# Kernel optimization log

Hardware: AMD Instinct MI355X
Metric: run time of the kernel (lower is better)

The kernel has to match this reference:

```python
import jax, jax.numpy as jnp
import numpy as np

NUM_HEADS = 16
NUM_KV_HEADS = 4
HEAD_DIM = 128
ROPE_BASE = 10000.0


def _apply_rope(x):
    # x: [B, H, S, D], interleaved RoPE: x1 = x[..., ::2], x2 = x[..., 1::2]
    B, H, S, D = x.shape
    inv_freq = 1.0 / (ROPE_BASE ** (jnp.arange(0, D, 2, dtype=jnp.float32) / D))  # [D/2]
    t = jnp.arange(S, dtype=jnp.float32)
    freqs = t[:, None] * inv_freq[None, :]          # [S, D/2]
    cos = jnp.cos(freqs)[None, None]                # [1,1,S,D/2]
    sin = jnp.sin(freqs)[None, None]
    xr = x.reshape(B, H, S, D // 2, 2)
    x1, x2 = xr[..., 0], xr[..., 1]
    r1 = x1 * cos - x2 * sin
    r2 = x1 * sin + x2 * cos
    return jnp.stack([r1, r2], axis=-1).reshape(B, H, S, D)


def setup_inputs() -> dict:
    key = jax.random.key(0)
    ks = jax.random.split(key, 5)
    H = NUM_HEADS * HEAD_DIM          # 2048
    KV = NUM_KV_HEADS * HEAD_DIM      # 512
    std = 0.02
    return {
        "hidden_states": jax.random.normal(ks[0], (1, 4096, H), dtype=jnp.float32),
        "wq": jax.random.normal(ks[1], (H, H), dtype=jnp.float32) * std,
        "wk": jax.random.normal(ks[2], (H, KV), dtype=jnp.float32) * std,
        "wv": jax.random.normal(ks[3], (H, KV), dtype=jnp.float32) * std,
        "wo": jax.random.normal(ks[4], (H, H), dtype=jnp.float32) * std,
    }


def reference(hidden_states, wq, wk, wv, wo):
    B, S, H = hidden_states.shape
    nh, nkv, hd = NUM_HEADS, NUM_KV_HEADS, HEAD_DIM
    scale = 1.0 / np.sqrt(hd)

    q = (hidden_states @ wq).reshape(B, S, nh, hd).transpose(0, 2, 1, 3)   # [B,nh,S,hd]
    k = (hidden_states @ wk).reshape(B, S, nkv, hd).transpose(0, 2, 1, 3)  # [B,nkv,S,hd]
    v = (hidden_states @ wv).reshape(B, S, nkv, hd).transpose(0, 2, 1, 3)

    q = _apply_rope(q)
    k = _apply_rope(k)

    rep = nh // nkv
    k = jnp.repeat(k, rep, axis=1)  # GQA head repetition -> [B,nh,S,hd]
    v = jnp.repeat(v, rep, axis=1)

    scores = jnp.einsum("bhqd,bhkd->bhqk", q, k) * scale
    causal = jnp.tril(jnp.ones((S, S), dtype=bool))
    scores = jnp.where(causal[None, None], scores, jnp.float32(-1e30))
    probs = jax.nn.softmax(scores, axis=-1)
    attn = jnp.einsum("bhqk,bhkd->bhqd", probs, v)      # [B,nh,S,hd]
    attn = attn.transpose(0, 2, 1, 3).reshape(B, S, H)
    return attn @ wo
```

## Files before the change

kernel.cpp:

```cpp
#include <hip/hip_runtime.h>

typedef unsigned short u16;
typedef unsigned int u32;
typedef __bf16 bf16x8 __attribute__((ext_vector_type(8)));
typedef float f32x4 __attribute__((ext_vector_type(4)));
typedef float f32x16 __attribute__((ext_vector_type(16)));
typedef int v2i __attribute__((ext_vector_type(2)));

#define S_LEN 4096
#define HDIM 2048
#define KVDIM 512
#define N_HEADS 16
#define HEAD_D 128

__device__ __forceinline__ u16 f2bf(float f) {
  u32 u = __float_as_uint(f);
  u32 r = (u + 0x7FFFu + ((u >> 16) & 1u)) >> 16;
  return (u16)r;
}
__device__ __forceinline__ float bf2f(u16 h) {
  return __uint_as_float(((u32)h) << 16);
}
__device__ __forceinline__ float exp2_fast(float x) {
  float r;
  asm("v_exp_f32 %0, %1" : "=v"(r) : "v"(x));
  return r;
}
__device__ __forceinline__ u32 cvt_pk_bf16(float lo, float hi) {
  u32 r;
  asm("v_cvt_pk_bf16_f32 %0, %1, %2" : "=v"(r) : "v"(lo), "v"(hi));
  return r;
}
__device__ __forceinline__ void gload16(const u16* g, const u16* l) {
  __builtin_amdgcn_global_load_lds(
      (const __attribute__((address_space(1))) void*)g,
      (__attribute__((address_space(3))) void*)l, 16, 0, 0);
}

__global__ void k_prep(const float* __restrict__ in, u16* __restrict__ out,
                       float* __restrict__ cosT, float* __restrict__ sinT) {
  int b = blockIdx.x;
  int tid = threadIdx.x;
  if (b < 4096) {
    int i = b * 256 + tid;
    const float4* p = reinterpret_cast<const float4*>(in) + (size_t)i * 2;
    float4 a = p[0], c = p[1];
    u32 o0 = (u32)f2bf(a.x) | ((u32)f2bf(a.y) << 16);
    u32 o1 = (u32)f2bf(a.z) | ((u32)f2bf(a.w) << 16);
    u32 o2 = (u32)f2bf(c.x) | ((u32)f2bf(c.y) << 16);
    u32 o3 = (u32)f2bf(c.z) | ((u32)f2bf(c.w) << 16);
    reinterpret_cast<uint4*>(out)[i] = make_uint4(o0, o1, o2, o3);
  } else {
    int i = (b - 4096) * 256 + tid;
    int pos = i >> 6, f = i & 63;
    float inv = expf(-0.1439115683121279f * (float)f);
    float ang = (float)pos * inv;
    float s, c;
    sincosf(ang, &s, &c);
    cosT[i] = c;
    sinT[i] = s;
  }
}

__global__ void k_transpose_all(const float* __restrict__ wq, const float* __restrict__ wk,
                                const float* __restrict__ wv, const float* __restrict__ wo,
                                u16* __restrict__ WqT, u16* __restrict__ WkT,
                                u16* __restrict__ WvT, u16* __restrict__ WoT) {
  __shared__ float t[32][33];
  int b = blockIdx.x;
  const float* W;
  u16* Wt;
  int Kd, Nd, bx, by;
  if (b < 4096) {
    W = wq; Wt = WqT; Kd = HDIM; Nd = HDIM; bx = b & 63; by = b >> 6;
  } else if (b < 5120) {
    int r = b - 4096; W = wk; Wt = WkT; Kd = HDIM; Nd = KVDIM; bx = r & 15; by = r >> 4;
  } else if (b < 6144) {
    int r = b - 5120; W = wv; Wt = WvT; Kd = HDIM; Nd = KVDIM; bx = r & 15; by = r >> 4;
  } else {
    int r = b - 6144; W = wo; Wt = WoT; Kd = HDIM; Nd = HDIM; bx = r & 63; by = r >> 6;
  }
  int tx = threadIdx.x & 31, ty = threadIdx.x >> 5;
  int n = bx * 32 + tx;
  for (int j = ty; j < 32; j += 8)
    t[j][tx] = W[(size_t)(by * 32 + j) * Nd + n];
  __syncthreads();
  int k = by * 32 + tx;
  for (int j = ty; j < 32; j += 8)
    Wt[(size_t)(bx * 32 + j) * Kd + k] = f2bf(t[tx][j]);
}

__global__ void k_rope_all(u16* __restrict__ Qb, u16* __restrict__ Kb,
                           const float* __restrict__ cosT, const float* __restrict__ sinT) {
  int b = blockIdx.x;
  u16* X;
  int width, i;
  if (b < 4096) { X = Qb; width = HDIM; i = b * 256 + threadIdx.x; }
  else { X = Kb; width = KVDIM; i = (b - 4096) * 256 + threadIdx.x; }
  size_t idx = (size_t)i * 8;
  int row = (int)(idx / width);
  int col = (int)(idx - (size_t)row * width);
  int fi = (col & 127) >> 1;
  float4 c4 = *reinterpret_cast<const float4*>(&cosT[(row << 6) + fi]);
  float4 s4 = *reinterpret_cast<const float4*>(&sinT[(row << 6) + fi]);
  uint4 v = *reinterpret_cast<const uint4*>(&X[idx]);
  float cc[4] = {c4.x, c4.y, c4.z, c4.w};
  float ss[4] = {s4.x, s4.y, s4.z, s4.w};
  u32 w_[4] = {v.x, v.y, v.z, v.w};
  u32 r_[4];
#pragma unroll
  for (int p = 0; p < 4; ++p) {
    float x1 = bf2f((u16)(w_[p] & 0xffff));
    float x2 = bf2f((u16)(w_[p] >> 16));
    float r1 = x1 * cc[p] - x2 * ss[p];
    float r2 = x1 * ss[p] + x2 * cc[p];
    r_[p] = (u32)f2bf(r1) | ((u32)f2bf(r2) << 16);
  }
  *reinterpret_cast<uint4*>(&X[idx]) = make_uint4(r_[0], r_[1], r_[2], r_[3]);
}

__global__ __launch_bounds__(256) void k_gemm_qkv(
    const u16* __restrict__ A, const u16* __restrict__ WqT, const u16* __restrict__ WkT,
    const u16* __restrict__ WvT, u16* __restrict__ Qb, u16* __restrict__ Kb,
    u16* __restrict__ VTb) {
  const int Kd = HDIM, M = S_LEN;
  __shared__ __align__(16) u16 As[128 * 32];
  __shared__ __align__(16) u16 Bs[128 * 32];
  const int p = blockIdx.x;
  const int bmg = p & 7, r = p >> 3;
  const int bm = (bmg * 4 + (r & 3)) * 128;
  const int by = r >> 2;
  const u16* Bt;
  int bn, N, mode;
  if (by < 16) { Bt = WqT; bn = by * 128; N = HDIM; mode = 0; }
  else if (by < 20) { Bt = WkT; bn = (by - 16) * 128; N = KVDIM; mode = 1; }
  else { Bt = WvT; bn = (by - 20) * 128; N = KVDIM; mode = 2; }
  const int tid = threadIdx.x;
  const int lane = tid & 63;
  const int wid = tid >> 6;
  const int wr = (wid >> 1) * 64, wc = (wid & 1) * 64;
  const int lr = lane & 15, lhi = lane >> 4;
  const int srow = lane >> 2;
  const int skc = (lane & 3) * 8;
  f32x4 acc[4][4] = {};
  for (int k0 = 0; k0 < Kd; k0 += 32) {
#pragma unroll
    for (int it = 0; it < 2; ++it) {
      int rowbase = (it * 4 + wid) * 16;
      gload16(&A[(size_t)(bm + rowbase + srow) * Kd + k0 + skc], &As[rowbase * 32]);
      gload16(&Bt[(size_t)(bn + rowbase + srow) * Kd + k0 + skc], &Bs[rowbase * 32]);
    }
    __syncthreads();
    bf16x8 af[4], bfr[4];
#pragma unroll
    for (int m = 0; m < 4; ++m)
      af[m] = *reinterpret_cast<const bf16x8*>(&As[(wr + m * 16 + lr) * 32 + lhi * 8]);
#pragma unroll
    for (int n = 0; n < 4; ++n)
      bfr[n] = *reinterpret_cast<const bf16x8*>(&Bs[(wc + n * 16 + lr) * 32 + lhi * 8]);
#pragma unroll
    for (int m = 0; m < 4; ++m)
#pragma unroll
      for (int n = 0; n < 4; ++n)
        acc[m][n] = __builtin_amdgcn_mfma_f32_16x16x32_bf16(af[m], bfr[n], acc[m][n], 0, 0, 0);
    __syncthreads();
  }
#pragma unroll
  for (int m = 0; m < 4; ++m) {
    int grow0 = bm + wr + m * 16 + lhi * 4;
#pragma unroll
    for (int n = 0; n < 4; ++n) {
      int gcol = bn + wc + n * 16 + lr;
      if (mode == 2) {
        ushort4 pk;
        pk.x = f2bf(acc[m][n][0]);
        pk.y = f2bf(acc[m][n][1]);
        pk.z = f2bf(acc[m][n][2]);
        pk.w = f2bf(acc[m][n][3]);
        *reinterpret_cast<ushort4*>(&VTb[(size_t)gcol * M + grow0]) = pk;
      } else {
        u16* outp = (mode == 0) ? Qb : Kb;
#pragma unroll
        for (int r2 = 0; r2 < 4; ++r2)
          outp[(size_t)(grow0 + r2) * N + gcol] = f2bf(acc[m][n][r2]);
      }
    }
  }
}

__global__ __launch_bounds__(256) void k_gemm_bt(
    const u16* __restrict__ A, const u16* __restrict__ Bt, float* __restrict__ Cout,
    int M, int N, int Kd) {
  __shared__ __align__(16) u16 As[128 * 32];
  __shared__ __align__(16) u16 Bs[128 * 32];
  const int p = blockIdx.x;
  const int bmg = p & 7, r = p >> 3;
  const int bm = (bmg * 4 + (r & 3)) * 128;
  const int bn = (r >> 2) * 128;
  const int tid = threadIdx.x;
  const int lane = tid & 63;
  const int wid = tid >> 6;
  const int wr = (wid >> 1) * 64, wc = (wid & 1) * 64;
  const int lr = lane & 15, lhi = lane >> 4;
  const int srow = lane >> 2;
  const int skc = (lane & 3) * 8;
  f32x4 acc[4][4] = {};
  for (int k0 = 0; k0 < Kd; k0 += 32) {
#pragma unroll
    for (int it = 0; it < 2; ++it) {
      int rowbase = (it * 4 + wid) * 16;
      gload16(&A[(size_t)(bm + rowbase + srow) * Kd + k0 + skc], &As[rowbase * 32]);
      gload16(&Bt[(size_t)(bn + rowbase + srow) * Kd + k0 + skc], &Bs[rowbase * 32]);
    }
    __syncthreads();
    bf16x8 af[4], bfr[4];
#pragma unroll
    for (int m = 0; m < 4; ++m)
      af[m] = *reinterpret_cast<const bf16x8*>(&As[(wr + m * 16 + lr) * 32 + lhi * 8]);
#pragma unroll
    for (int n = 0; n < 4; ++n)
      bfr[n] = *reinterpret_cast<const bf16x8*>(&Bs[(wc + n * 16 + lr) * 32 + lhi * 8]);
#pragma unroll
    for (int m = 0; m < 4; ++m)
#pragma unroll
      for (int n = 0; n < 4; ++n)
        acc[m][n] = __builtin_amdgcn_mfma_f32_16x16x32_bf16(af[m], bfr[n], acc[m][n], 0, 0, 0);
    __syncthreads();
  }
#pragma unroll
  for (int m = 0; m < 4; ++m) {
    int grow0 = bm + wr + m * 16 + lhi * 4;
#pragma unroll
    for (int n = 0; n < 4; ++n) {
      int gcol = bn + wc + n * 16 + lr;
#pragma unroll
      for (int r2 = 0; r2 < 4; ++r2)
        Cout[(size_t)(grow0 + r2) * N + gcol] = acc[m][n][r2];
    }
  }
}

__global__ __launch_bounds__(256, 2) void k_attn(
    const u16* __restrict__ Q, const u16* __restrict__ K, const u16* __restrict__ VT,
    u16* __restrict__ PO0, u16* __restrict__ PO1, float2* __restrict__ ML) {
  __shared__ __align__(16) u16 Ks[64 * 128];
  __shared__ __align__(16) u16 Vs[128 * 64];
  int i = blockIdx.x;
  const int x = i & 7, s = i >> 3;
  const int kvh = x >> 1;
  const int kvhalf = x & 1;
  const int hp = s & 3;
  const int u = s >> 2;
  const int g = u & 7, jq = u >> 3;
  int qt;
  if (jq == 0) qt = g;
  else if (jq == 1) qt = 15 - g;
  else if (jq == 2) qt = 16 + g;
  else qt = 31 - g;
  const int h = kvh * 4 + hp;
  const int tid = threadIdx.x, lane = tid & 63, wid = tid >> 6;
  const int l31 = lane & 31, hi = lane >> 5;
  const int qw = qt * 128 + wid * 32;
  const int qglob = qw + l31;
  const float CE = 0.12751743f;
  const float THR = 62.74f;

  const u16* qptr = &Q[(size_t)qglob * HDIM + h * HEAD_D];
  bf16x8 qf[8];
#pragma unroll
  for (int ks = 0; ks < 8; ++ks)
    qf[ks] = *reinterpret_cast<const bf16x8*>(&qptr[ks * 16 + hi * 8]);

  f32x16 o_[4] = {};
  float m_ = -3e38f, l_ = 0.f;
  char* KsB = (char*)Ks;
  char* VsB = (char*)Vs;

  const int j0 = kvhalf * (qt + 1);
  const int j1 = j0 + qt + 1;
  for (int j = j0; j < j1; ++j) {
    const int kb = j << 6;
    __syncthreads();
#pragma unroll
    for (int it = 0; it < 4; ++it) {
      int sI = it * 256 + tid;
      int kv = sI >> 4, c16 = sI & 15;
      int db = kv * 256 + c16 * 16;
      db ^= ((db >> 8) & 7) << 4;
      *reinterpret_cast<uint4*>(KsB + db) = *reinterpret_cast<const uint4*>(
          &K[(size_t)(kb + kv) * KVDIM + kvh * HEAD_D + c16 * 8]);
    }
#pragma unroll
    for (int it = 0; it < 4; ++it) {
      int sI = it * 256 + tid;
      int d = sI >> 3, k16 = sI & 7;
      int db = d * 128 + k16 * 16;
      db ^= ((db >> 7) & 7) << 4;
      *reinterpret_cast<uint4*>(VsB + db) = *reinterpret_cast<const uint4*>(
          &VT[(size_t)(kvh * HEAD_D + d) * S_LEN + kb + k16 * 8]);
    }
    __syncthreads();

    if (kb <= qw + 31) {
      f32x16 s0 = {}, s1 = {};
#pragma unroll
      for (int ks = 0; ks < 8; ++ks) {
        int db0 = l31 * 256 + ks * 32 + hi * 16;
        db0 ^= ((db0 >> 8) & 7) << 4;
        int db1 = (32 + l31) * 256 + ks * 32 + hi * 16;
        db1 ^= ((db1 >> 8) & 7) << 4;
        bf16x8 k0 = *reinterpret_cast<const bf16x8*>(KsB + db0);
        bf16x8 k1 = *reinterpret_cast<const bf16x8*>(KsB + db1);
        s0 = __builtin_amdgcn_mfma_f32_32x32x16_bf16(k0, qf[ks], s0, 0, 0, 0);
        s1 = __builtin_amdgcn_mfma_f32_32x32x16_bf16(k1, qf[ks], s1, 0, 0, 0);
      }
      if (kb + 63 > qw) {
#pragma unroll
        for (int r = 0; r < 16; ++r) {
          int kvr = kb + (r & 3) + 8 * (r >> 2) + 4 * hi;
          if (kvr > qglob) s0[r] = -1e30f;
          if (kvr + 32 > qglob) s1[r] = -1e30f;
        }
      }
      float pm = fmaxf(s0[0], s1[0]);
#pragma unroll
      for (int r = 1; r < 16; ++r) pm = fmaxf(pm, fmaxf(s0[r], s1[r]));
      pm = fmaxf(pm, __shfl_xor(pm, 32));
      if (!__all(pm <= m_ + THR)) {
        float mnew = fmaxf(m_, pm);
        float fac = exp2_fast((m_ - mnew) * CE);
        m_ = mnew;
        l_ *= fac;
#pragma unroll
        for (int dt = 0; dt < 4; ++dt)
#pragma unroll
          for (int r = 0; r < 16; ++r) o_[dt][r] *= fac;
      }
      const float mc = m_ * CE;
      float rs = 0.f;
#pragma unroll
      for (int r = 0; r < 16; ++r) {
        s0[r] = exp2_fast(__builtin_fmaf(s0[r], CE, -mc));
        s1[r] = exp2_fast(__builtin_fmaf(s1[r], CE, -mc));
        rs += s0[r] + s1[r];
      }
      rs += __shfl_xor(rs, 32);
      l_ += rs;
#pragma unroll
      for (int kvt = 0; kvt < 2; ++kvt) {
        u32 xw[8], yw[8];
#pragma unroll
        for (int gI = 0; gI < 8; ++gI) {
          float plo = kvt ? s1[2 * gI] : s0[2 * gI];
          float phi = kvt ? s1[2 * gI + 1] : s0[2 * gI + 1];
          u32 pw = cvt_pk_bf16(plo, phi);
          v2i sw = __builtin_amdgcn_permlane32_swap((int)pw, (int)pw, false, false);
          xw[gI] = (u32)sw[0];
          yw[gI] = (u32)sw[1];
        }
#pragma unroll
        for (int ksl = 0; ksl < 2; ++ksl) {
          int b = ksl * 4;
          u32 f0 = hi ? xw[b + 2] : xw[b + 0];
          u32 f1 = hi ? xw[b + 3] : xw[b + 1];
          u32 f2 = hi ? yw[b + 2] : yw[b + 0];
          u32 f3 = hi ? yw[b + 3] : yw[b + 1];
          uint4 fr = make_uint4(f0, f1, f2, f3);
          bf16x8 pf = *reinterpret_cast<bf16x8*>(&fr);
          const int kvstep = kvt * 2 + ksl;
#pragma unroll
          for (int dt = 0; dt < 4; ++dt) {
            int db = (dt * 32 + l31) * 128 + kvstep * 32 + hi * 16;
            db ^= ((db >> 7) & 7) << 4;
            bf16x8 vf = *reinterpret_cast<const bf16x8*>(VsB + db);
            o_[dt] = __builtin_amdgcn_mfma_f32_32x32x16_bf16(vf, pf, o_[dt], 0, 0, 0);
          }
        }
      }
    }
  }
  const float inv_l = (l_ > 0.f) ? (1.0f / l_) : 0.f;
  u16* PO = kvhalf ? PO1 : PO0;
  u16* optr = &PO[(size_t)qglob * HDIM + h * HEAD_D];
#pragma unroll
  for (int dt = 0; dt < 4; ++dt)
#pragma unroll
    for (int gI = 0; gI < 4; ++gI) {
      ushort4 pk;
      pk.x = f2bf(o_[dt][4 * gI + 0] * inv_l);
      pk.y = f2bf(o_[dt][4 * gI + 1] * inv_l);
      pk.z = f2bf(o_[dt][4 * gI + 2] * inv_l);
      pk.w = f2bf(o_[dt][4 * gI + 3] * inv_l);
      *reinterpret_cast<ushort4*>(&optr[dt * 32 + gI * 8 + hi * 4]) = pk;
    }
  if (hi == 0)
    ML[(size_t)kvhalf * N_HEADS * S_LEN + (size_t)h * S_LEN + qglob] =
        make_float2(m_, l_);
}

__global__ void k_combine(const u16* __restrict__ PO0, const u16* __restrict__ PO1,
                          const float2* __restrict__ ML, u16* __restrict__ Out) {
  int i = blockIdx.x * 256 + threadIdx.x;
  int d8 = (i & 15) * 8;
  int qh = i >> 4;
  int h = qh & 15, q = qh >> 4;
  const float CE = 0.12751743f;
  float2 ml1 = ML[(size_t)h * S_LEN + q];
  float2 ml2 = ML[(size_t)N_HEADS * S_LEN + (size_t)h * S_LEN + q];
  float m = fmaxf(ml1.x, ml2.x);
  float w1 = ml1.y * exp2_fast((ml1.x - m) * CE);
  float w2 = ml2.y * exp2_fast((ml2.x - m) * CE);
  float inv = 1.0f / (w1 + w2);
  w1 *= inv;
  w2 *= inv;
  size_t base = (size_t)q * HDIM + h * HEAD_D + d8;
  uint4 a = *reinterpret_cast<const uint4*>(&PO0[base]);
  uint4 b = *reinterpret_cast<const uint4*>(&PO1[base]);
  u32 aw[4] = {a.x, a.y, a.z, a.w}, bw[4] = {b.x, b.y, b.z, b.w};
  u32 ow[4];
#pragma unroll
  for (int p = 0; p < 4; ++p) {
    float lo = w1 * bf2f((u16)(aw[p] & 0xffff)) + w2 * bf2f((u16)(bw[p] & 0xffff));
    float hi2 = w1 * bf2f((u16)(aw[p] >> 16)) + w2 * bf2f((u16)(bw[p] >> 16));
    ow[p] = (u32)f2bf(lo) | ((u32)f2bf(hi2) << 16);
  }
  *reinterpret_cast<uint4*>(&Out[base]) = make_uint4(ow[0], ow[1], ow[2], ow[3]);
}

extern "C" void kernel_launch(void* const* d_in, const int* in_sizes, int n_in,
                              void* d_out, int out_size, void* d_ws, size_t ws_size,
                              hipStream_t stream) {
  const float* hs = (const float*)d_in[0];
  const float* wq = (const float*)d_in[1];
  const float* wk = (const float*)d_in[2];
  const float* wv = (const float*)d_in[3];
  const float* wo = (const float*)d_in[4];

  char* ws = (char*)d_ws;
  size_t off = 0;
  auto alloc = [&](size_t bytes) {
    void* p = ws + off;
    off += (bytes + 255) & ~(size_t)255;
    return p;
  };
  u16* Xb = (u16*)alloc((size_t)S_LEN * HDIM * 2);
  u16* WqT = (u16*)alloc((size_t)HDIM * HDIM * 2);
  u16* WkT = (u16*)alloc((size_t)KVDIM * HDIM * 2);
  u16* WvT = (u16*)alloc((size_t)KVDIM * HDIM * 2);
  u16* WoT = (u16*)alloc((size_t)HDIM * HDIM * 2);
  u16* Qb = (u16*)alloc((size_t)S_LEN * HDIM * 2);
  u16* Kb = (u16*)alloc((size_t)S_LEN * KVDIM * 2);
  u16* VTb = (u16*)alloc((size_t)KVDIM * S_LEN * 2);
  u16* Ab = (u16*)alloc((size_t)S_LEN * HDIM * 2);
  float* cosT = (float*)alloc((size_t)S_LEN * 64 * 4);
  float* sinT = (float*)alloc((size_t)S_LEN * 64 * 4);
  if (off > ws_size) return;

  u16* PO0 = Ab;
  u16* PO1 = Xb;
  float2* ML = (float2*)WqT;

  k_prep<<<dim3(5120), dim3(256), 0, stream>>>(hs, Xb, cosT, sinT);
  k_transpose_all<<<dim3(10240), dim3(256), 0, stream>>>(wq, wk, wv, wo, WqT, WkT, WvT, WoT);
  k_gemm_qkv<<<dim3(768), dim3(256), 0, stream>>>(Xb, WqT, WkT, WvT, Qb, Kb, VTb);
  k_rope_all<<<dim3(5120), dim3(256), 0, stream>>>(Qb, Kb, cosT, sinT);
  k_attn<<<dim3(1024), dim3(256), 0, stream>>>(Qb, Kb, VTb, PO0, PO1, ML);
  k_combine<<<dim3(4096), dim3(256), 0, stream>>>(PO0, PO1, ML, Ab);
  k_gemm_bt<<<dim3(512), dim3(256), 0, stream>>>(Ab, WoT, (float*)d_out, S_LEN, HDIM, HDIM);
}
```

Before: 275.8 us.

## Double GEMM K-tile to 64 and XOR-swizzle LDS layout in projection GEMMs

Both the QKV projection GEMM and the output projection GEMM now stage a 64-wide K slice per iteration instead of 32. This halves the number of barrier pairs and loop iterations. Global-to-LDS loads are remapped so each thread loads a 16-byte chunk, and the chunk column is XOR-swizzled by row to reduce LDS bank conflicts on the fragment reads. LDS use per block doubles, which may lower occupancy, and there is still no double buffering.

```diff
diff --git a/kernel.cpp b/kernel.cpp
--- a/kernel.cpp
+++ b/kernel.cpp
@@ -124,8 +124,8 @@
     const u16* __restrict__ WvT, u16* __restrict__ Qb, u16* __restrict__ Kb,
     u16* __restrict__ VTb) {
   const int Kd = HDIM, M = S_LEN;
-  __shared__ __align__(16) u16 As[128 * 32];
-  __shared__ __align__(16) u16 Bs[128 * 32];
+  __shared__ __align__(16) u16 As[128 * 64];
+  __shared__ __align__(16) u16 Bs[128 * 64];
   const int p = blockIdx.x;
   const int bmg = p & 7, r = p >> 3;
   const int bm = (bmg * 4 + (r & 3)) * 128;
@@ -140,29 +140,38 @@
   const int wid = tid >> 6;
   const int wr = (wid >> 1) * 64, wc = (wid & 1) * 64;
   const int lr = lane & 15, lhi = lane >> 4;
-  const int srow = lane >> 2;
-  const int skc = (lane & 3) * 8;
   f32x4 acc[4][4] = {};
-  for (int k0 = 0; k0 < Kd; k0 += 32) {
-#pragma unroll
-    for (int it = 0; it < 2; ++it) {
-      int rowbase = (it * 4 + wid) * 16;
-      gload16(&A[(size_t)(bm + rowbase + srow) * Kd + k0 + skc], &As[rowbase * 32]);
-      gload16(&Bt[(size_t)(bn + rowbase + srow) * Kd + k0 + skc], &Bs[rowbase * 32]);
-    }
-    __syncthreads();
-    bf16x8 af[4], bfr[4];
-#pragma unroll
-    for (int m = 0; m < 4; ++m)
-      af[m] = *reinterpret_cast<const bf16x8*>(&As[(wr + m * 16 + lr) * 32 + lhi * 8]);
-#pragma unroll
-    for (int n = 0; n < 4; ++n)
-      bfr[n] = *reinterpret_cast<const bf16x8*>(&Bs[(wc + n * 16 + lr) * 32 + lhi * 8]);
-#pragma unroll
-    for (int m = 0; m < 4; ++m)
-#pragma unroll
-      for (int n = 0; n < 4; ++n)
-        acc[m][n] = __builtin_amdgcn_mfma_f32_16x16x32_bf16(af[m], bfr[n], acc[m][n], 0, 0, 0);
+  for (int k0 = 0; k0 < Kd; k0 += 64) {
+#pragma unroll
+    for (int it = 0; it < 4; ++it) {
+      int s = it * 256 + tid;
+      int row = s >> 3, c = s & 7;
+      int sc = (c ^ (row & 7)) * 8;
+      gload16(&A[(size_t)(bm + row) * Kd + k0 + sc], &As[s * 8]);
+      gload16(&Bt[(size_t)(bn + row) * Kd + k0 + sc], &Bs[s * 8]);
+    }
+    __syncthreads();
+#pragma unroll
+    for (int kk = 0; kk < 2; ++kk) {
+      bf16x8 af[4], bfr[4];
+#pragma unroll
+      for (int m = 0; m < 4; ++m) {
+        int row = wr + m * 16 + lr;
+        int rc = (kk * 4 + lhi) ^ (row & 7);
+        af[m] = *reinterpret_cast<const bf16x8*>(&As[row * 64 + rc * 8]);
+      }
+#pragma unroll
+      for (int n = 0; n < 4; ++n) {
+        int row = wc + n * 16 + lr;
+        int rc = (kk * 4 + lhi) ^ (row & 7);
+        bfr[n] = *reinterpret_cast<const bf16x8*>(&Bs[row * 64 + rc * 8]);
+      }
+#pragma unroll
+      for (int m = 0; m < 4; ++m)
+#pragma unroll
+        for (int n = 0; n < 4; ++n)
+          acc[m][n] = __builtin_amdgcn_mfma_f32_16x16x32_bf16(af[m], bfr[n], acc[m][n], 0, 0, 0);
+    }
     __syncthreads();
   }
 #pragma unroll
@@ -191,8 +200,8 @@
 __global__ __launch_bounds__(256) void k_gemm_bt(
     const u16* __restrict__ A, const u16* __restrict__ Bt, float* __restrict__ Cout,
     int M, int N, int Kd) {
-  __shared__ __align__(16) u16 As[128 * 32];
-  __shared__ __align__(16) u16 Bs[128 * 32];
+  __shared__ __align__(16) u16 As[128 * 64];
+  __shared__ __align__(16) u16 Bs[128 * 64];
   const int p = blockIdx.x;
   const int bmg = p & 7, r = p >> 3;
   const int bm = (bmg * 4 + (r & 3)) * 128;
@@ -202,29 +211,38 @@
   const int wid = tid >> 6;
   const int wr = (wid >> 1) * 64, wc = (wid & 1) * 64;
   const int lr = lane & 15, lhi = lane >> 4;
-  const int srow = lane >> 2;
-  const int skc = (lane & 3) * 8;
   f32x4 acc[4][4] = {};
-  for (int k0 = 0; k0 < Kd; k0 += 32) {
-#pragma unroll
-    for (int it = 0; it < 2; ++it) {
-      int rowbase = (it * 4 + wid) * 16;
-      gload16(&A[(size_t)(bm + rowbase + srow) * Kd + k0 + skc], &As[rowbase * 32]);
-      gload16(&Bt[(size_t)(bn + rowbase + srow) * Kd + k0 + skc], &Bs[rowbase * 32]);
-    }
-    __syncthreads();
-    bf16x8 af[4], bfr[4];
-#pragma unroll
-    for (int m = 0; m < 4; ++m)
-      af[m] = *reinterpret_cast<const bf16x8*>(&As[(wr + m * 16 + lr) * 32 + lhi * 8]);
-#pragma unroll
-    for (int n = 0; n < 4; ++n)
-      bfr[n] = *reinterpret_cast<const bf16x8*>(&Bs[(wc + n * 16 + lr) * 32 + lhi * 8]);
-#pragma unroll
-    for (int m = 0; m < 4; ++m)
-#pragma unroll
-      for (int n = 0; n < 4; ++n)
-        acc[m][n] = __builtin_amdgcn_mfma_f32_16x16x32_bf16(af[m], bfr[n], acc[m][n], 0, 0, 0);
+  for (int k0 = 0; k0 < Kd; k0 += 64) {
+#pragma unroll
+    for (int it = 0; it < 4; ++it) {
+      int s = it * 256 + tid;
+      int row = s >> 3, c = s & 7;
+      int sc = (c ^ (row & 7)) * 8;
+      gload16(&A[(size_t)(bm + row) * Kd + k0 + sc], &As[s * 8]);
+      gload16(&Bt[(size_t)(bn + row) * Kd + k0 + sc], &Bs[s * 8]);
+    }
+    __syncthreads();
+#pragma unroll
+    for (int kk = 0; kk < 2; ++kk) {
+      bf16x8 af[4], bfr[4];
+#pragma unroll
+      for (int m = 0; m < 4; ++m) {
+        int row = wr + m * 16 + lr;
+        int rc = (kk * 4 + lhi) ^ (row & 7);
+        af[m] = *reinterpret_cast<const bf16x8*>(&As[row * 64 + rc * 8]);
+      }
+#pragma unroll
+      for (int n = 0; n < 4; ++n) {
+        int row = wc + n * 16 + lr;
+        int rc = (kk * 4 + lhi) ^ (row & 7);
+        bfr[n] = *reinterpret_cast<const bf16x8*>(&Bs[row * 64 + rc * 8]);
+      }
+#pragma unroll
+      for (int m = 0; m < 4; ++m)
+#pragma unroll
+        for (int n = 0; n < 4; ++n)
+          acc[m][n] = __builtin_amdgcn_mfma_f32_16x16x32_bf16(af[m], bfr[n], acc[m][n], 0, 0, 0);
+    }
     __syncthreads();
   }
 #pragma unroll
```

New measurement: 271.7 us. No clear change (-1.5%).
